# Kernel tuning notes

Hardware: AMD Instinct MI355X
Metric: run time of the kernel (lower is better)

Reference implementation:

```python
import jax, jax.numpy as jnp
import numpy as np

B, P, C, H, W = 2048, 50, 512, 7, 8


def setup_inputs() -> dict:
    key = jax.random.key(0)
    k1, k2 = jax.random.split(key)
    x = jax.random.normal(k1, (B, C, H, W), dtype=jnp.float32)
    # nn.init.xavier_uniform_ on (P, C, H, W) -> small-scale init
    prototype = jax.random.normal(k2, (P, C, H, W), dtype=jnp.float32) * 0.02
    return {"x": x, "prototype": prototype}


def reference(x, prototype):
    """PrototypeLayer euclidean branch.

    Torch original:
      x2_sum = conv2d(x**2, ones_like(prototype))   # full-size kernel -> [B,P,1,1], same value per p
      p2     = sum(prototype**2, dims=(1,2,3)).view(1,P,1,1)
      xp     = conv2d(x, prototype)                  # [B,P,1,1]
      dist   = relu(x2_sum + p2 - 2*xp).view(B,P)
    The full-size-kernel convs reduce to global sums / a [B,P] contraction.
    """
    x2_sum = jnp.sum(x * x, axis=(1, 2, 3))                 # [B]
    p2 = jnp.sum(prototype * prototype, axis=(1, 2, 3))     # [P]
    xp = jnp.einsum('bchw,pchw->bp', x, prototype)          # [B,P]
    distance = jax.nn.relu(x2_sum[:, None] + p2[None, :] - 2.0 * xp)
    return distance
```

## Files before the change

kernel.cpp:

```cpp
#include <hip/hip_runtime.h>
#include <hip/hip_bf16.h>


typedef __bf16 bf16_t;
typedef bf16_t bf16x8 __attribute__((ext_vector_type(8)));
typedef bf16_t bf16x4 __attribute__((ext_vector_type(4)));
typedef float  floatx4 __attribute__((ext_vector_type(4)));

#define KDIM 28672
#define BDIM 2048
#define KSPLIT 32
#define KCHUNK (KDIM / KSPLIT)
#define STEPS (KCHUNK / 32)

__global__ __launch_bounds__(256) void proto_prep(const float* __restrict__ proto,
                                                  bf16_t* __restrict__ pb,
                                                  float* __restrict__ p2) {
    int p = blockIdx.x;
    int t = threadIdx.x;
    float acc = 0.f;
    if (p < 50) {
        const floatx4* src = (const floatx4*)(proto + (long)p * KDIM);
        for (int i = t; i < KDIM / 4; i += 256) {
            floatx4 v = src[i];
            acc += v[0]*v[0] + v[1]*v[1] + v[2]*v[2] + v[3]*v[3];
            bf16x4 o;
            o[0] = (bf16_t)v[0]; o[1] = (bf16_t)v[1];
            o[2] = (bf16_t)v[2]; o[3] = (bf16_t)v[3];
            *(bf16x4*)(pb + (long)p * KDIM + i * 4) = o;
        }
    } else {
        bf16x4 z;
        z[0] = (bf16_t)0.f; z[1] = (bf16_t)0.f; z[2] = (bf16_t)0.f; z[3] = (bf16_t)0.f;
        for (int i = t; i < KDIM / 4; i += 256)
            *(bf16x4*)(pb + (long)p * KDIM + i * 4) = z;
    }
    __shared__ float sred[256];
    sred[t] = acc;
    __syncthreads();
    for (int s = 128; s > 0; s >>= 1) {
        if (t < s) sred[t] += sred[t + s];
        __syncthreads();
    }
    if (t == 0) p2[p] = (p < 50) ? sred[0] : 0.f;
}

__global__ __launch_bounds__(256, 4) void proto_main(const float* __restrict__ x,
                                                     const bf16_t* __restrict__ pb,
                                                     float* __restrict__ xpp,
                                                     float* __restrict__ x2p) {
    const int t = threadIdx.x;
    const int lane = t & 63;
    const int wave = t >> 6;
    const int lr = lane & 15;
    const int quad = lane >> 4;
    const int mbase = blockIdx.x * 64;
    const int ks = blockIdx.y;
    const int kbase = ks * KCHUNK;

    const int mrow = mbase + wave * 16 + lr;
    const float* xr = x + (long)mrow * KDIM + kbase + quad * 8;
    const bf16_t* pr0 = pb + (long)(0  + lr) * KDIM + kbase + quad * 8;
    const bf16_t* pr1 = pb + (long)(16 + lr) * KDIM + kbase + quad * 8;
    const bf16_t* pr2 = pb + (long)(32 + lr) * KDIM + kbase + quad * 8;
    const bf16_t* pr3 = pb + (long)(48 + lr) * KDIM + kbase + quad * 8;

    floatx4 acc0 = {0.f,0.f,0.f,0.f};
    floatx4 acc1 = {0.f,0.f,0.f,0.f};
    floatx4 acc2 = {0.f,0.f,0.f,0.f};
    floatx4 acc3 = {0.f,0.f,0.f,0.f};
    float x2acc = 0.f;

    floatx4 a0 = *(const floatx4*)(xr);
    floatx4 a1 = *(const floatx4*)(xr + 4);
    bf16x8 b0 = *(const bf16x8*)(pr0);
    bf16x8 b1 = *(const bf16x8*)(pr1);
    bf16x8 b2 = *(const bf16x8*)(pr2);
    bf16x8 b3 = *(const bf16x8*)(pr3);

    for (int it = 0; it < STEPS; ++it) {
        const int nk = (it + 1 < STEPS ? it + 1 : 0) * 32;
        floatx4 na0 = *(const floatx4*)(xr + nk);
        floatx4 na1 = *(const floatx4*)(xr + nk + 4);
        bf16x8 nb0 = *(const bf16x8*)(pr0 + nk);
        bf16x8 nb1 = *(const bf16x8*)(pr1 + nk);
        bf16x8 nb2 = *(const bf16x8*)(pr2 + nk);
        bf16x8 nb3 = *(const bf16x8*)(pr3 + nk);

        x2acc += a0[0]*a0[0] + a0[1]*a0[1] + a0[2]*a0[2] + a0[3]*a0[3]
               + a1[0]*a1[0] + a1[1]*a1[1] + a1[2]*a1[2] + a1[3]*a1[3];
        bf16x8 av;
        av[0] = (bf16_t)a0[0]; av[1] = (bf16_t)a0[1];
        av[2] = (bf16_t)a0[2]; av[3] = (bf16_t)a0[3];
        av[4] = (bf16_t)a1[0]; av[5] = (bf16_t)a1[1];
        av[6] = (bf16_t)a1[2]; av[7] = (bf16_t)a1[3];

        acc0 = __builtin_amdgcn_mfma_f32_16x16x32_bf16(av, b0, acc0, 0, 0, 0);
        acc1 = __builtin_amdgcn_mfma_f32_16x16x32_bf16(av, b1, acc1, 0, 0, 0);
        acc2 = __builtin_amdgcn_mfma_f32_16x16x32_bf16(av, b2, acc2, 0, 0, 0);
        acc3 = __builtin_amdgcn_mfma_f32_16x16x32_bf16(av, b3, acc3, 0, 0, 0);

        a0 = na0; a1 = na1;
        b0 = nb0; b1 = nb1; b2 = nb2; b3 = nb3;
    }

    x2acc += __shfl_xor(x2acc, 16, 64);
    x2acc += __shfl_xor(x2acc, 32, 64);
    if (quad == 0)
        x2p[ks * BDIM + mbase + wave * 16 + lr] = x2acc;

    const long base = ((long)ks * BDIM + mbase + wave * 16) * 64;
    #pragma unroll
    for (int r = 0; r < 4; ++r) {
        const int mr = quad * 4 + r;
        xpp[base + (long)mr * 64 + 0  + lr] = acc0[r];
        xpp[base + (long)mr * 64 + 16 + lr] = acc1[r];
        xpp[base + (long)mr * 64 + 32 + lr] = acc2[r];
        xpp[base + (long)mr * 64 + 48 + lr] = acc3[r];
    }
}

__global__ __launch_bounds__(256) void proto_finalize(const float* __restrict__ xpp,
                                                      const float* __restrict__ x2p,
                                                      const float* __restrict__ p2,
                                                      float* __restrict__ out) {
    int idx = blockIdx.x * 256 + threadIdx.x;
    int b = idx >> 6;
    int n = idx & 63;
    if (n >= 50) return;
    float xp = 0.f, x2 = 0.f;
    #pragma unroll
    for (int ksi = 0; ksi < KSPLIT; ++ksi) {
        xp += xpp[((long)ksi * BDIM + b) * 64 + n];
        x2 += x2p[ksi * BDIM + b];
    }
    float d = x2 + p2[n] - 2.f * xp;
    out[b * 50 + n] = d > 0.f ? d : 0.f;
}

extern "C" void kernel_launch(void* const* d_in, const int* in_sizes, int n_in,
                              void* d_out, int out_size, void* d_ws, size_t ws_size,
                              hipStream_t stream) {
    const float* x = (const float*)d_in[0];
    const float* proto = (const float*)d_in[1];
    float* out = (float*)d_out;

    char* ws = (char*)d_ws;
    bf16_t* pb  = (bf16_t*)(ws);
    float*  p2  = (float*)(ws + 3670016);
    float*  x2p = (float*)(ws + 3670272);
    float*  xpp = (float*)(ws + 3932416);

    proto_prep<<<64, 256, 0, stream>>>(proto, pb, p2);
    proto_main<<<dim3(32, KSPLIT), 256, 0, stream>>>(x, pb, xpp, x2p);
    proto_finalize<<<(BDIM * 64) / 256, 256, 0, stream>>>(xpp, x2p, p2, out);
}
```

Measured before the change: 366.5 us.

## Stage bf16-converted x tile in double-buffered LDS with 2x2 wave tiling

```diff
diff --git a/kernel.cpp b/kernel.cpp
--- a/kernel.cpp
+++ b/kernel.cpp
@@ -11,7 +11,8 @@
 #define BDIM 2048
 #define KSPLIT 32
 #define KCHUNK (KDIM / KSPLIT)
-#define STEPS (KCHUNK / 32)
+#define STEPS (KCHUNK / 64)
+#define ASTRIDE 72
 
 __global__ __launch_bounds__(256) void proto_prep(const float* __restrict__ proto,
                                                   bf16_t* __restrict__ pb,
@@ -49,74 +50,125 @@
                                                      const bf16_t* __restrict__ pb,
                                                      float* __restrict__ xpp,
                                                      float* __restrict__ x2p) {
+    __shared__ bf16_t As[2][64 * ASTRIDE];
+
     const int t = threadIdx.x;
     const int lane = t & 63;
     const int wave = t >> 6;
     const int lr = lane & 15;
-    const int quad = lane >> 4;
+    const int q  = lane >> 4;
     const int mbase = blockIdx.x * 64;
     const int ks = blockIdx.y;
     const int kbase = ks * KCHUNK;
 
-    const int mrow = mbase + wave * 16 + lr;
-    const float* xr = x + (long)mrow * KDIM + kbase + quad * 8;
-    const bf16_t* pr0 = pb + (long)(0  + lr) * KDIM + kbase + quad * 8;
-    const bf16_t* pr1 = pb + (long)(16 + lr) * KDIM + kbase + quad * 8;
-    const bf16_t* pr2 = pb + (long)(32 + lr) * KDIM + kbase + quad * 8;
-    const bf16_t* pr3 = pb + (long)(48 + lr) * KDIM + kbase + quad * 8;
-
-    floatx4 acc0 = {0.f,0.f,0.f,0.f};
-    floatx4 acc1 = {0.f,0.f,0.f,0.f};
-    floatx4 acc2 = {0.f,0.f,0.f,0.f};
-    floatx4 acc3 = {0.f,0.f,0.f,0.f};
+    const int srow = t >> 2;
+    const int sq   = t & 3;
+    const float* xrow = x + (long)(mbase + srow) * KDIM + kbase + sq * 16;
+    bf16_t* const awr[2] = { &As[0][srow * ASTRIDE + sq * 16],
+                             &As[1][srow * ASTRIDE + sq * 16] };
+
+    const int m0 = (wave >> 1) * 32;
+    const int n0 = (wave & 1) * 32;
+    const bf16_t* pbr0 = pb + (long)(n0 + lr) * KDIM + kbase + q * 8;
+    const bf16_t* pbr1 = pb + (long)(n0 + 16 + lr) * KDIM + kbase + q * 8;
+    const int ard0 = (m0 + lr) * ASTRIDE + q * 8;
+    const int ard1 = (m0 + 16 + lr) * ASTRIDE + q * 8;
+
+    floatx4 acc00 = {0.f,0.f,0.f,0.f};
+    floatx4 acc01 = {0.f,0.f,0.f,0.f};
+    floatx4 acc10 = {0.f,0.f,0.f,0.f};
+    floatx4 acc11 = {0.f,0.f,0.f,0.f};
     float x2acc = 0.f;
 
-    floatx4 a0 = *(const floatx4*)(xr);
-    floatx4 a1 = *(const floatx4*)(xr + 4);
-    bf16x8 b0 = *(const bf16x8*)(pr0);
-    bf16x8 b1 = *(const bf16x8*)(pr1);
-    bf16x8 b2 = *(const bf16x8*)(pr2);
-    bf16x8 b3 = *(const bf16x8*)(pr3);
-
+    floatx4 c0 = *(const floatx4*)(xrow);
+    floatx4 c1 = *(const floatx4*)(xrow + 4);
+    floatx4 c2 = *(const floatx4*)(xrow + 8);
+    floatx4 c3 = *(const floatx4*)(xrow + 12);
+    {
+        x2acc += c0[0]*c0[0] + c0[1]*c0[1] + c0[2]*c0[2] + c0[3]*c0[3]
+               + c1[0]*c1[0] + c1[1]*c1[1] + c1[2]*c1[2] + c1[3]*c1[3]
+               + c2[0]*c2[0] + c2[1]*c2[1] + c2[2]*c2[2] + c2[3]*c2[3]
+               + c3[0]*c3[0] + c3[1]*c3[1] + c3[2]*c3[2] + c3[3]*c3[3];
+        bf16x8 lo, hi;
+        lo[0]=(bf16_t)c0[0]; lo[1]=(bf16_t)c0[1]; lo[2]=(bf16_t)c0[2]; lo[3]=(bf16_t)c0[3];
+        lo[4]=(bf16_t)c1[0]; lo[5]=(bf16_t)c1[1]; lo[6]=(bf16_t)c1[2]; lo[7]=(bf16_t)c1[3];
+        hi[0]=(bf16_t)c2[0]; hi[1]=(bf16_t)c2[1]; hi[2]=(bf16_t)c2[2]; hi[3]=(bf16_t)c2[3];
+        hi[4]=(bf16_t)c3[0]; hi[5]=(bf16_t)c3[1]; hi[6]=(bf16_t)c3[2]; hi[7]=(bf16_t)c3[3];
+        *(bf16x8*)(awr[0])     = lo;
+        *(bf16x8*)(awr[0] + 8) = hi;
+    }
+    c0 = *(const floatx4*)(xrow + 64);
+    c1 = *(const floatx4*)(xrow + 68);
+    c2 = *(const floatx4*)(xrow + 72);
+    c3 = *(const floatx4*)(xrow + 76);
+    __syncthreads();
+
+    #pragma unroll 2
     for (int it = 0; it < STEPS; ++it) {
-        const int nk = (it + 1 < STEPS ? it + 1 : 0) * 32;
-        floatx4 na0 = *(const floatx4*)(xr + nk);
-        floatx4 na1 = *(const floatx4*)(xr + nk + 4);
-        bf16x8 nb0 = *(const bf16x8*)(pr0 + nk);
-        bf16x8 nb1 = *(const bf16x8*)(pr1 + nk);
-        bf16x8 nb2 = *(const bf16x8*)(pr2 + nk);
-        bf16x8 nb3 = *(const bf16x8*)(pr3 + nk);
-
-        x2acc += a0[0]*a0[0] + a0[1]*a0[1] + a0[2]*a0[2] + a0[3]*a0[3]
-               + a1[0]*a1[0] + a1[1]*a1[1] + a1[2]*a1[2] + a1[3]*a1[3];
-        bf16x8 av;
-        av[0] = (bf16_t)a0[0]; av[1] = (bf16_t)a0[1];
-        av[2] = (bf16_t)a0[2]; av[3] = (bf16_t)a0[3];
-        av[4] = (bf16_t)a1[0]; av[5] = (bf16_t)a1[1];
-        av[6] = (bf16_t)a1[2]; av[7] = (bf16_t)a1[3];
-
-        acc0 = __builtin_amdgcn_mfma_f32_16x16x32_bf16(av, b0, acc0, 0, 0, 0);
-        acc1 = __builtin_amdgcn_mfma_f32_16x16x32_bf16(av, b1, acc1, 0, 0, 0);
-        acc2 = __builtin_amdgcn_mfma_f32_16x16x32_bf16(av, b2, acc2, 0, 0, 0);
-        acc3 = __builtin_amdgcn_mfma_f32_16x16x32_bf16(av, b3, acc3, 0, 0, 0);
-
-        a0 = na0; a1 = na1;
-        b0 = nb0; b1 = nb1; b2 = nb2; b3 = nb3;
-    }
-
-    x2acc += __shfl_xor(x2acc, 16, 64);
-    x2acc += __shfl_xor(x2acc, 32, 64);
-    if (quad == 0)
-        x2p[ks * BDIM + mbase + wave * 16 + lr] = x2acc;
-
-    const long base = ((long)ks * BDIM + mbase + wave * 16) * 64;
+        const int buf = it & 1;
+
+        const int ko = it * 64;
+        bf16x8 b00 = *(const bf16x8*)(pbr0 + ko);
+        bf16x8 b01 = *(const bf16x8*)(pbr0 + ko + 32);
+        bf16x8 b10 = *(const bf16x8*)(pbr1 + ko);
+        bf16x8 b11 = *(const bf16x8*)(pbr1 + ko + 32);
+
+        const int nk = (it + 2 < STEPS ? it + 2 : STEPS - 1) * 64;
+        floatx4 n0v = *(const floatx4*)(xrow + nk);
+        floatx4 n1v = *(const floatx4*)(xrow + nk + 4);
+        floatx4 n2v = *(const floatx4*)(xrow + nk + 8);
+        floatx4 n3v = *(const floatx4*)(xrow + nk + 12);
+
+        if (it + 1 < STEPS) {
+            x2acc += c0[0]*c0[0] + c0[1]*c0[1] + c0[2]*c0[2] + c0[3]*c0[3]
+                   + c1[0]*c1[0] + c1[1]*c1[1] + c1[2]*c1[2] + c1[3]*c1[3]
+                   + c2[0]*c2[0] + c2[1]*c2[1] + c2[2]*c2[2] + c2[3]*c2[3]
+                   + c3[0]*c3[0] + c3[1]*c3[1] + c3[2]*c3[2] + c3[3]*c3[3];
+            bf16x8 lo, hi;
+            lo[0]=(bf16_t)c0[0]; lo[1]=(bf16_t)c0[1]; lo[2]=(bf16_t)c0[2]; lo[3]=(bf16_t)c0[3];
+            lo[4]=(bf16_t)c1[0]; lo[5]=(bf16_t)c1[1]; lo[6]=(bf16_t)c1[2]; lo[7]=(bf16_t)c1[3];
+            hi[0]=(bf16_t)c2[0]; hi[1]=(bf16_t)c2[1]; hi[2]=(bf16_t)c2[2]; hi[3]=(bf16_t)c2[3];
+            hi[4]=(bf16_t)c3[0]; hi[5]=(bf16_t)c3[1]; hi[6]=(bf16_t)c3[2]; hi[7]=(bf16_t)c3[3];
+            *(bf16x8*)(awr[buf ^ 1])     = lo;
+            *(bf16x8*)(awr[buf ^ 1] + 8) = hi;
+        }
+
+        {
+            const bf16_t* ab = &As[buf][0];
+            bf16x8 a00 = *(const bf16x8*)(ab + ard0);
+            bf16x8 a01 = *(const bf16x8*)(ab + ard0 + 32);
+            bf16x8 a10 = *(const bf16x8*)(ab + ard1);
+            bf16x8 a11 = *(const bf16x8*)(ab + ard1 + 32);
+            acc00 = __builtin_amdgcn_mfma_f32_16x16x32_bf16(a00, b00, acc00, 0, 0, 0);
+            acc10 = __builtin_amdgcn_mfma_f32_16x16x32_bf16(a10, b00, acc10, 0, 0, 0);
+            acc01 = __builtin_amdgcn_mfma_f32_16x16x32_bf16(a00, b10, acc01, 0, 0, 0);
+            acc11 = __builtin_amdgcn_mfma_f32_16x16x32_bf16(a10, b10, acc11, 0, 0, 0);
+            acc00 = __builtin_amdgcn_mfma_f32_16x16x32_bf16(a01, b01, acc00, 0, 0, 0);
+            acc10 = __builtin_amdgcn_mfma_f32_16x16x32_bf16(a11, b01, acc10, 0, 0, 0);
+            acc01 = __builtin_amdgcn_mfma_f32_16x16x32_bf16(a01, b11, acc01, 0, 0, 0);
+            acc11 = __builtin_amdgcn_mfma_f32_16x16x32_bf16(a11, b11, acc11, 0, 0, 0);
+        }
+
+        __syncthreads();
+        c0 = n0v; c1 = n1v; c2 = n2v; c3 = n3v;
+    }
+
+    const long base = ((long)ks * BDIM + mbase) * 64;
     #pragma unroll
     for (int r = 0; r < 4; ++r) {
-        const int mr = quad * 4 + r;
-        xpp[base + (long)mr * 64 + 0  + lr] = acc0[r];
-        xpp[base + (long)mr * 64 + 16 + lr] = acc1[r];
-        xpp[base + (long)mr * 64 + 32 + lr] = acc2[r];
-        xpp[base + (long)mr * 64 + 48 + lr] = acc3[r];
+        const int mr = m0 + q * 4 + r;
+        xpp[base + (long)mr * 64 + n0 + lr]             = acc00[r];
+        xpp[base + (long)mr * 64 + n0 + 16 + lr]        = acc01[r];
+        xpp[base + (long)(mr + 16) * 64 + n0 + lr]      = acc10[r];
+        xpp[base + (long)(mr + 16) * 64 + n0 + 16 + lr] = acc11[r];
+    }
+
+    float* red = (float*)&As[0][0];
+    red[t] = x2acc;
+    __syncthreads();
+    if (t < 64) {
+        float s = red[4 * t] + red[4 * t + 1] + red[4 * t + 2] + red[4 * t + 3];
+        x2p[ks * BDIM + mbase + t] = s;
     }
 }
 
```

Result: faster. 350.8 us (-4.3%).
